# Optimization experiments

Hardware: AMD Instinct MI355X
Metric: run time of the kernel (lower is better)

Reference implementation:

```python
import jax, jax.numpy as jnp
import numpy as np
import math

D_MODEL = 1024
NHEAD = 16
SEQ_LEN = 4096
K_PROJ = 16
HEAD_DIM = D_MODEL // NHEAD


def setup_inputs() -> dict:
    key = jax.random.key(0)
    ks = jax.random.split(key, 11)
    x = jax.random.normal(ks[0], (4, SEQ_LEN, D_MODEL), dtype=jnp.float32)
    s = 1.0 / math.sqrt(D_MODEL)
    Wq = jax.random.uniform(ks[1], (D_MODEL, D_MODEL), minval=-s, maxval=s)
    bq = jax.random.uniform(ks[2], (D_MODEL,), minval=-s, maxval=s)
    Wk = jax.random.uniform(ks[3], (D_MODEL, D_MODEL), minval=-s, maxval=s)
    bk = jax.random.uniform(ks[4], (D_MODEL,), minval=-s, maxval=s)
    Wv = jax.random.uniform(ks[5], (D_MODEL, D_MODEL), minval=-s, maxval=s)
    bv = jax.random.uniform(ks[6], (D_MODEL,), minval=-s, maxval=s)
    Wo = jax.random.uniform(ks[7], (D_MODEL, D_MODEL), minval=-s, maxval=s)
    bo = jax.random.uniform(ks[8], (D_MODEL,), minval=-s, maxval=s)
    E = jax.random.normal(ks[9], (NHEAD, K_PROJ, SEQ_LEN)) * 0.02
    F = jax.random.normal(ks[10], (NHEAD, K_PROJ, SEQ_LEN)) * 0.02
    return {"x": x, "Wq": Wq, "bq": bq, "Wk": Wk, "bk": bk,
            "Wv": Wv, "bv": bv, "Wo": Wo, "bo": bo, "E": E, "F": F}


def reference(x, Wq, bq, Wk, bk, Wv, bv, Wo, bo, E, F):
    B, N, D = x.shape
    # torch Linear: y = x @ W.T + b
    q = x @ Wq.T + bq
    k = x @ Wk.T + bk
    v = x @ Wv.T + bv
    # [B, H, N, Dh]
    def split_heads(t):
        return t.reshape(B, N, NHEAD, HEAD_DIM).transpose(0, 2, 1, 3)
    q, k, v = split_heads(q), split_heads(k), split_heads(v)
    # low-rank projections of K, V along sequence: [B, H, Kp, Dh]
    k_lin = jnp.einsum('bhnd,hkn->bhkd', k, E)
    v_lin = jnp.einsum('bhnd,hkn->bhkd', v, F)
    scores = jnp.einsum('bhnd,bhkd->bhnk', q, k_lin) / math.sqrt(HEAD_DIM)
    attn = jax.nn.softmax(scores, axis=-1)  # dropout is identity in eval
    out = jnp.einsum('bhnk,bhkd->bhnd', attn, v_lin)
    out = out.transpose(0, 2, 1, 3).reshape(B, N, D)
    return out @ Wo.T + bo
```

## Files before the change

### kernel.cpp

```cpp
#include <hip/hip_runtime.h>
#include <hip/hip_bf16.h>

#define SEQLEN 4096

typedef __bf16 bf16x8 __attribute__((ext_vector_type(8)));
typedef float f32x4 __attribute__((ext_vector_type(4)));
typedef __attribute__((ext_vector_type(8))) unsigned short u16x8;

__device__ inline float bf2f(unsigned short s) {
  union { unsigned u; float f; } t; t.u = ((unsigned)s) << 16; return t.f;
}
__device__ inline unsigned short f2bf(float f) {
  __hip_bfloat16 h = __float2bfloat16(f);
  return *reinterpret_cast<unsigned short*>(&h);
}

__device__ inline void gload_lds16(const void* g, void* l) {
  __builtin_amdgcn_global_load_lds(
      (const __attribute__((address_space(1))) unsigned int*)g,
      (__attribute__((address_space(3))) unsigned int*)l, 16, 0, 0);
}

__global__ void cvt_f32_to_bf16(const float* __restrict__ s,
                                unsigned short* __restrict__ d, int n4) {
  int i = blockIdx.x * 256 + threadIdx.x;
  if (i >= n4) return;
  float4 v = reinterpret_cast<const float4*>(s)[i];
  ushort4 o;
  o.x = f2bf(v.x); o.y = f2bf(v.y); o.z = f2bf(v.z); o.w = f2bf(v.w);
  reinterpret_cast<ushort4*>(d)[i] = o;
}

__global__ void pack_bias(const float* __restrict__ a, const float* __restrict__ b,
                          const float* __restrict__ c, float* __restrict__ dst) {
  int i = blockIdx.x * 256 + threadIdx.x;
  if (i < 1024) { dst[i] = a[i]; dst[1024 + i] = b[i]; dst[2048 + i] = c[i]; }
}


#define MFMA16(mk, A00, A01, A10, A11)                                          \
  __builtin_amdgcn_s_setprio(1);                                                \
  _Pragma("unroll")                                                             \
  for (int n = 0; n < 4; ++n) {                                                 \
    acc[2*(mk)][n]   = __builtin_amdgcn_mfma_f32_16x16x32_bf16(A00, b[n][0], acc[2*(mk)][n],   0, 0, 0); \
    acc[2*(mk)][n]   = __builtin_amdgcn_mfma_f32_16x16x32_bf16(A01, b[n][1], acc[2*(mk)][n],   0, 0, 0); \
    acc[2*(mk)+1][n] = __builtin_amdgcn_mfma_f32_16x16x32_bf16(A10, b[n][0], acc[2*(mk)+1][n], 0, 0, 0); \
    acc[2*(mk)+1][n] = __builtin_amdgcn_mfma_f32_16x16x32_bf16(A11, b[n][1], acc[2*(mk)+1][n], 0, 0, 0); \
  }                                                                             \
  __builtin_amdgcn_s_setprio(0);

#define LDA8(mi, sg) (*reinterpret_cast<const bf16x8*>(&as[((wr << 7) + (mi) * 16 + r16) * 64 + (sg) * 8]))
#define LDB8(ni, sg) (*reinterpret_cast<const bf16x8*>(&bs[((wc << 6) + (ni) * 16 + r16) * 64 + (sg) * 8]))

template <typename OUT_T>
__global__ __launch_bounds__(512, 2) void gemm8p(
    const unsigned short* __restrict__ A, const unsigned short* __restrict__ B,
    const float* __restrict__ bias, OUT_T* __restrict__ C, int M, int N, int K,
    int ldc) {
  extern __shared__ __align__(16) unsigned short lds[];

  const int tid = threadIdx.x;
  const int lane = tid & 63, wv = tid >> 6;
  const int wr = wv >> 2, wc = wv & 3;
  const int r16 = lane & 15, kg = lane >> 4;
  const int sg0 = (0 * 4 + kg) ^ (r16 & 7);
  const int sg1 = (1 * 4 + kg) ^ (r16 & 7);

  const int nwg = gridDim.x;
  const int cpx = nwg >> 3;
  const int swz = ((int)blockIdx.x & 7) * cpx + ((int)blockIdx.x >> 3);
  const int mt = M >> 8;
  const int tile_m = swz % mt, tile_n = swz / mt;
  const int brow = tile_m << 8, bcol = tile_n << 8;

  const unsigned short* Ag = A + (size_t)brow * K;
  const unsigned short* Bg = B + (size_t)bcol * K;

  const int sr = tid >> 3;
  const int sc = tid & 7;
  const int sgl = sc ^ (sr & 7);

  auto STG = [&](const unsigned short* G, unsigned short* dstbuf, int row0, int kt) {
    gload_lds16(G + (size_t)(row0 + sr) * K + (size_t)kt * 64 + sgl * 8,
                dstbuf + (row0 + sr) * 64 + sc * 8);
  };

  f32x4 acc[8][4];
#pragma unroll
  for (int m = 0; m < 8; ++m)
#pragma unroll
    for (int n = 0; n < 4; ++n) acc[m][n] = (f32x4)0.0f;

  {
    unsigned short* a0 = lds;
    unsigned short* b0 = lds + 32768;
    STG(Bg, b0, 0, 0);   STG(Bg, b0, 64, 0);
    STG(Bg, b0, 128, 0); STG(Bg, b0, 192, 0);
    STG(Ag, a0, 0, 0);   STG(Ag, a0, 128, 0);
    STG(Ag, a0, 64, 0);  STG(Ag, a0, 192, 0);
  }
  asm volatile("s_waitcnt vmcnt(2)" ::: "memory");
  __builtin_amdgcn_s_barrier();

  const int NT = K >> 6;
  for (int t = 0; t < NT; ++t) {
    const int cur = t & 1;
    const unsigned short* as = lds + (cur << 14);
    const unsigned short* bs = lds + 32768 + (cur << 14);
    unsigned short* an = lds + ((cur ^ 1) << 14);
    unsigned short* bn = lds + 32768 + ((cur ^ 1) << 14);
    const int tn = (t + 1 < NT) ? t + 1 : 0;

    bf16x8 b[4][2];
#pragma unroll
    for (int n = 0; n < 4; ++n) { b[n][0] = LDB8(n, sg0); b[n][1] = LDB8(n, sg1); }

    {
      bf16x8 a00 = LDA8(0, sg0), a01 = LDA8(0, sg1);
      bf16x8 a10 = LDA8(1, sg0), a11 = LDA8(1, sg1);
      STG(Bg, bn, 0, tn);   STG(Bg, bn, 64, tn);
      STG(Bg, bn, 128, tn); STG(Bg, bn, 192, tn);
      __builtin_amdgcn_s_barrier();
      MFMA16(0, a00, a01, a10, a11);
      __builtin_amdgcn_s_barrier();
    }
    {
      bf16x8 a00 = LDA8(2, sg0), a01 = LDA8(2, sg1);
      bf16x8 a10 = LDA8(3, sg0), a11 = LDA8(3, sg1);
      STG(Ag, an, 0, tn); STG(Ag, an, 128, tn);
      __builtin_amdgcn_s_barrier();
      MFMA16(1, a00, a01, a10, a11);
      asm volatile("s_waitcnt vmcnt(6)" ::: "memory");
      __builtin_amdgcn_s_barrier();
    }
    {
      bf16x8 a00 = LDA8(4, sg0), a01 = LDA8(4, sg1);
      bf16x8 a10 = LDA8(5, sg0), a11 = LDA8(5, sg1);
      STG(Ag, an, 64, tn); STG(Ag, an, 192, tn);
      __builtin_amdgcn_s_barrier();
      MFMA16(2, a00, a01, a10, a11);
      __builtin_amdgcn_s_barrier();
    }
    {
      bf16x8 a00 = LDA8(6, sg0), a01 = LDA8(6, sg1);
      bf16x8 a10 = LDA8(7, sg0), a11 = LDA8(7, sg1);
      __builtin_amdgcn_s_barrier();
      MFMA16(3, a00, a01, a10, a11);
      asm volatile("s_waitcnt vmcnt(2)" ::: "memory");
      __builtin_amdgcn_s_barrier();
    }
  }
  asm volatile("s_waitcnt vmcnt(0)" ::: "memory");

  if constexpr (sizeof(OUT_T) == 2) {
    __builtin_amdgcn_s_barrier();
    unsigned short* C2 = reinterpret_cast<unsigned short*>(C);
    float bvs[4];
#pragma unroll
    for (int n = 0; n < 4; ++n)
      bvs[n] = bias ? bias[bcol + wc * 64 + n * 16 + r16] : 0.0f;
#pragma unroll
    for (int m = 0; m < 8; ++m) {
#pragma unroll
      for (int r = 0; r < 4; ++r) {
        int rw = m * 16 + kg * 4 + r;
        int xo = (rw & 12) << 2;
#pragma unroll
        for (int n = 0; n < 4; ++n) {
          lds[wv * 8192 + rw * 64 + ((n * 16 + r16) ^ xo)] =
              f2bf(acc[m][n][r] + bvs[n]);
        }
      }
    }
    __syncthreads();
#pragma unroll
    for (int p = 0; p < 16; ++p) {
      int grow = p * 16 + (tid >> 5);
      int g = tid & 31;
      int wvs = ((grow >> 7) << 2) + (g >> 3);
      int row_l = grow & 127;
      int src = wvs * 8192 + row_l * 64 + (((g & 7) * 8) ^ ((row_l & 12) << 2));
      u16x8 vv = *reinterpret_cast<const u16x8*>(&lds[src]);
      *reinterpret_cast<u16x8*>(&C2[(size_t)(brow + grow) * ldc + bcol + g * 8]) = vv;
    }
  } else {
#pragma unroll
    for (int n = 0; n < 4; ++n) {
      int col = bcol + wc * 64 + n * 16 + r16;
      float bv = bias ? bias[col] : 0.0f;
#pragma unroll
      for (int m = 0; m < 8; ++m) {
#pragma unroll
        for (int r = 0; r < 4; ++r) {
          int row = brow + wr * 128 + m * 16 + kg * 4 + r;
          C[(size_t)row * ldc + col] = acc[m][n][r] + bv;
        }
      }
    }
  }
}

__global__ void kvlin_part(const unsigned short* __restrict__ qkv,
                           const float* __restrict__ E, const float* __restrict__ F,
                           float* __restrict__ part) {
  __shared__ __align__(16) unsigned short Ks[128 * 64], Vs[128 * 64];
  __shared__ __align__(16) float Es[16 * 128], Fs[16 * 128];
  const int tid = threadIdx.x;
  const int bid = blockIdx.x;
  const int bh = bid >> 3, ns = bid & 7;
  const int b = bh >> 4, h = bh & 15;
  const int d = tid & 63, kk = tid >> 6;
  float aK[4] = {0, 0, 0, 0}, aV[4] = {0, 0, 0, 0};
  for (int c = 0; c < 4; ++c) {
    int n0 = ns * 512 + c * 128;
#pragma unroll
    for (int it = 0; it < 4; ++it) {
      int f = it * 256 + tid;
      int row = f >> 3, ch = f & 7;
      const unsigned short* gk =
          qkv + (size_t)(b * SEQLEN + n0 + row) * 3072 + 1024 + h * 64 + ch * 8;
      gload_lds16(gk, &Ks[f * 8]);
      gload_lds16(gk + 1024, &Vs[f * 8]);
    }
#pragma unroll
    for (int it = 0; it < 2; ++it) {
      int f = it * 256 + tid;
      int k = f >> 5, ch = f & 31;
      const float* ge = E + (size_t)(h * 16 + k) * SEQLEN + n0 + ch * 4;
      const float* gf = F + (size_t)(h * 16 + k) * SEQLEN + n0 + ch * 4;
      gload_lds16(ge, &Es[f * 4]);
      gload_lds16(gf, &Fs[f * 4]);
    }
    __syncthreads();
    for (int n = 0; n < 128; ++n) {
      float kv = bf2f(Ks[n * 64 + d]);
      float vv = bf2f(Vs[n * 64 + d]);
#pragma unroll
      for (int j = 0; j < 4; ++j) {
        aK[j] += Es[(kk * 4 + j) * 128 + n] * kv;
        aV[j] += Fs[(kk * 4 + j) * 128 + n] * vv;
      }
    }
    __syncthreads();
  }
  size_t base = ((size_t)ns * 64 + bh) * 2048;
#pragma unroll
  for (int j = 0; j < 4; ++j) {
    part[base + (kk * 4 + j) * 64 + d] = aK[j];
    part[base + 1024 + (kk * 4 + j) * 64 + d] = aV[j];
  }
}

__global__ void kvlin_reduce(const float* __restrict__ part, float* __restrict__ out) {
  int i = blockIdx.x * 256 + threadIdx.x;
  float s = 0;
#pragma unroll
  for (int ns = 0; ns < 8; ++ns) s += part[(size_t)ns * 131072 + i];
  out[i] = s;
}

__global__ void attn_kernel(const unsigned short* __restrict__ qkv,
                            const float* __restrict__ kvlin,
                            unsigned short* __restrict__ aout) {
  __shared__ float kl[1024], vl[1024];
  const int tid = threadIdx.x;
  const int bid = blockIdx.x;
  const int bh = bid >> 4, nt = bid & 15;
  const int b = bh >> 4, h = bh & 15;
  for (int i = tid; i < 1024; i += 256) {
    kl[i] = kvlin[(size_t)bh * 2048 + i];
    vl[i] = kvlin[(size_t)bh * 2048 + 1024 + i];
  }
  __syncthreads();
  const int n = nt * 256 + tid;
  const unsigned short* qp = qkv + (size_t)(b * SEQLEN + n) * 3072 + h * 64;
  float q[64];
#pragma unroll
  for (int c2 = 0; c2 < 8; ++c2) {
    u16x8 v = *reinterpret_cast<const u16x8*>(qp + c2 * 8);
#pragma unroll
    for (int j = 0; j < 8; ++j) q[c2 * 8 + j] = bf2f(v[j]);
  }
  float s[16];
#pragma unroll
  for (int k = 0; k < 16; ++k) {
    float a = 0;
#pragma unroll
    for (int dd = 0; dd < 64; ++dd) a += q[dd] * kl[k * 64 + dd];
    s[k] = a * 0.125f;
  }
  float mx = s[0];
#pragma unroll
  for (int k = 1; k < 16; ++k) mx = fmaxf(mx, s[k]);
  float sum = 0;
#pragma unroll
  for (int k = 0; k < 16; ++k) { s[k] = __expf(s[k] - mx); sum += s[k]; }
  float inv = 1.0f / sum;
#pragma unroll
  for (int k = 0; k < 16; ++k) s[k] *= inv;
  unsigned short* op = aout + (size_t)(b * SEQLEN + n) * 1024 + h * 64;
#pragma unroll
  for (int d0 = 0; d0 < 8; ++d0) {
    float o[8] = {0, 0, 0, 0, 0, 0, 0, 0};
#pragma unroll
    for (int k = 0; k < 16; ++k) {
      float p = s[k];
#pragma unroll
      for (int j = 0; j < 8; ++j) o[j] += p * vl[k * 64 + d0 * 8 + j];
    }
    u16x8 pk;
#pragma unroll
    for (int j = 0; j < 8; ++j) pk[j] = f2bf(o[j]);
    *reinterpret_cast<u16x8*>(op + d0 * 8) = pk;
  }
}

extern "C" void kernel_launch(void* const* d_in, const int* in_sizes, int n_in,
                              void* d_out, int out_size, void* d_ws, size_t ws_size,
                              hipStream_t stream) {
  const float* x  = (const float*)d_in[0];
  const float* Wq = (const float*)d_in[1];
  const float* bq = (const float*)d_in[2];
  const float* Wk = (const float*)d_in[3];
  const float* bk = (const float*)d_in[4];
  const float* Wv = (const float*)d_in[5];
  const float* bv = (const float*)d_in[6];
  const float* Wo = (const float*)d_in[7];
  const float* bo = (const float*)d_in[8];
  const float* E  = (const float*)d_in[9];
  const float* F  = (const float*)d_in[10];
  float* out = (float*)d_out;

  char* ws = (char*)d_ws;
  unsigned short* Xb   = (unsigned short*)(ws);
  unsigned short* Wqkv = (unsigned short*)(ws + 33554432);
  unsigned short* WoB  = (unsigned short*)(ws + 39845888);
  float*          Bqkv = (float*)(ws + 41943040);
  unsigned short* QKV  = (unsigned short*)(ws + 41955328);
  float*          KVp  = (float*)(ws + 142618624);
  float*          KVl  = (float*)(ws + 146812928);
  unsigned short* AOut = Xb;

  (void)hipFuncSetAttribute(reinterpret_cast<const void*>(gemm8p<unsigned short>),
                            hipFuncAttributeMaxDynamicSharedMemorySize, 131072);
  (void)hipFuncSetAttribute(reinterpret_cast<const void*>(gemm8p<float>),
                            hipFuncAttributeMaxDynamicSharedMemorySize, 131072);

  cvt_f32_to_bf16<<<16384, 256, 0, stream>>>(x, Xb, 4194304);
  cvt_f32_to_bf16<<<1024, 256, 0, stream>>>(Wq, Wqkv, 262144);
  cvt_f32_to_bf16<<<1024, 256, 0, stream>>>(Wk, Wqkv + 1048576, 262144);
  cvt_f32_to_bf16<<<1024, 256, 0, stream>>>(Wv, Wqkv + 2097152, 262144);
  cvt_f32_to_bf16<<<1024, 256, 0, stream>>>(Wo, WoB, 262144);
  pack_bias<<<4, 256, 0, stream>>>(bq, bk, bv, Bqkv);

  gemm8p<unsigned short><<<768, 512, 131072, stream>>>(
      Xb, Wqkv, Bqkv, QKV, 16384, 3072, 1024, 3072);

  kvlin_part<<<512, 256, 0, stream>>>(QKV, E, F, KVp);
  kvlin_reduce<<<512, 256, 0, stream>>>(KVp, KVl);
  attn_kernel<<<1024, 256, 0, stream>>>(QKV, KVl, AOut);

  gemm8p<float><<<256, 512, 131072, stream>>>(
      AOut, WoB, bo, out, 16384, 1024, 1024, 1024);
}
```

Baseline: 266.8 us.

## Fuse conversion kernels, reorder MFMA issue, and remap GEMM tiles per XCD

Merges the five fp32-to-bf16 conversion launches and the bias packing into one kernel, removing several small launches and their gaps. Reorders the MFMA sequence in the GEMM inner macro so that consecutive instructions write different accumulators, which may reduce dependency stalls. Changes the block-to-tile mapping so each XCD handles a contiguous band of M tiles, aiming for better L2 reuse of A rows. The fused kernel adds branching, and the new mapping assumes M/256 is divisible by 8.

```diff
diff --git a/kernel.cpp b/kernel.cpp
--- a/kernel.cpp
+++ b/kernel.cpp
@@ -21,32 +21,59 @@
       (__attribute__((address_space(3))) unsigned int*)l, 16, 0, 0);
 }
 
-__global__ void cvt_f32_to_bf16(const float* __restrict__ s,
-                                unsigned short* __restrict__ d, int n4) {
-  int i = blockIdx.x * 256 + threadIdx.x;
-  if (i >= n4) return;
-  float4 v = reinterpret_cast<const float4*>(s)[i];
+__global__ void cvt_all(const float* __restrict__ x, const float* __restrict__ Wq,
+                        const float* __restrict__ Wk, const float* __restrict__ Wv,
+                        const float* __restrict__ Wo,
+                        const float* __restrict__ bq, const float* __restrict__ bk,
+                        const float* __restrict__ bv,
+                        unsigned short* __restrict__ Xb,
+                        unsigned short* __restrict__ Wqkv,
+                        unsigned short* __restrict__ WoB, float* __restrict__ Bqkv) {
+  long i = (long)blockIdx.x * 256 + threadIdx.x;
+  const float* src;
+  unsigned short* dst;
+  long rel;
+  if (i < 4194304) {
+    src = x; dst = Xb; rel = i;
+  } else if (i < 4456448) {
+    src = Wq; dst = Wqkv; rel = i - 4194304;
+  } else if (i < 4718592) {
+    src = Wk; dst = Wqkv + 1048576; rel = i - 4456448;
+  } else if (i < 4980736) {
+    src = Wv; dst = Wqkv + 2097152; rel = i - 4718592;
+  } else if (i < 5242880) {
+    src = Wo; dst = WoB; rel = i - 4980736;
+  } else if (i < 5243648) {
+    long j = i - 5242880;
+    const float* bsrc = (j < 256) ? bq : (j < 512) ? bk : bv;
+    long jr = j & 255;
+    reinterpret_cast<float4*>(Bqkv)[j] =
+        reinterpret_cast<const float4*>(bsrc)[jr];
+    return;
+  } else {
+    return;
+  }
+  float4 v = reinterpret_cast<const float4*>(src)[rel];
   ushort4 o;
   o.x = f2bf(v.x); o.y = f2bf(v.y); o.z = f2bf(v.z); o.w = f2bf(v.w);
-  reinterpret_cast<ushort4*>(d)[i] = o;
-}
-
-__global__ void pack_bias(const float* __restrict__ a, const float* __restrict__ b,
-                          const float* __restrict__ c, float* __restrict__ dst) {
-  int i = blockIdx.x * 256 + threadIdx.x;
-  if (i < 1024) { dst[i] = a[i]; dst[1024 + i] = b[i]; dst[2048 + i] = c[i]; }
+  reinterpret_cast<ushort4*>(dst)[rel] = o;
 }
 
 
 #define MFMA16(mk, A00, A01, A10, A11)                                          \
   __builtin_amdgcn_s_setprio(1);                                                \
   _Pragma("unroll")                                                             \
-  for (int n = 0; n < 4; ++n) {                                                 \
+  for (int n = 0; n < 4; ++n)                                                   \
     acc[2*(mk)][n]   = __builtin_amdgcn_mfma_f32_16x16x32_bf16(A00, b[n][0], acc[2*(mk)][n],   0, 0, 0); \
+  _Pragma("unroll")                                                             \
+  for (int n = 0; n < 4; ++n)                                                   \
+    acc[2*(mk)+1][n] = __builtin_amdgcn_mfma_f32_16x16x32_bf16(A10, b[n][0], acc[2*(mk)+1][n], 0, 0, 0); \
+  _Pragma("unroll")                                                             \
+  for (int n = 0; n < 4; ++n)                                                   \
     acc[2*(mk)][n]   = __builtin_amdgcn_mfma_f32_16x16x32_bf16(A01, b[n][1], acc[2*(mk)][n],   0, 0, 0); \
-    acc[2*(mk)+1][n] = __builtin_amdgcn_mfma_f32_16x16x32_bf16(A10, b[n][0], acc[2*(mk)+1][n], 0, 0, 0); \
+  _Pragma("unroll")                                                             \
+  for (int n = 0; n < 4; ++n)                                                   \
     acc[2*(mk)+1][n] = __builtin_amdgcn_mfma_f32_16x16x32_bf16(A11, b[n][1], acc[2*(mk)+1][n], 0, 0, 0); \
-  }                                                                             \
   __builtin_amdgcn_s_setprio(0);
 
 #define LDA8(mi, sg) (*reinterpret_cast<const bf16x8*>(&as[((wr << 7) + (mi) * 16 + r16) * 64 + (sg) * 8]))
@@ -66,11 +93,11 @@
   const int sg0 = (0 * 4 + kg) ^ (r16 & 7);
   const int sg1 = (1 * 4 + kg) ^ (r16 & 7);
 
-  const int nwg = gridDim.x;
-  const int cpx = nwg >> 3;
-  const int swz = ((int)blockIdx.x & 7) * cpx + ((int)blockIdx.x >> 3);
-  const int mt = M >> 8;
-  const int tile_m = swz % mt, tile_n = swz / mt;
+  const int xcd = (int)blockIdx.x & 7;
+  const int pos = (int)blockIdx.x >> 3;
+  const int rpx = (M >> 8) >> 3;
+  const int tile_m = xcd * rpx + (pos % rpx);
+  const int tile_n = pos / rpx;
   const int brow = tile_m << 8, bcol = tile_n << 8;
 
   const unsigned short* Ag = A + (size_t)brow * K;
@@ -346,12 +373,8 @@
   (void)hipFuncSetAttribute(reinterpret_cast<const void*>(gemm8p<float>),
                             hipFuncAttributeMaxDynamicSharedMemorySize, 131072);
 
-  cvt_f32_to_bf16<<<16384, 256, 0, stream>>>(x, Xb, 4194304);
-  cvt_f32_to_bf16<<<1024, 256, 0, stream>>>(Wq, Wqkv, 262144);
-  cvt_f32_to_bf16<<<1024, 256, 0, stream>>>(Wk, Wqkv + 1048576, 262144);
-  cvt_f32_to_bf16<<<1024, 256, 0, stream>>>(Wv, Wqkv + 2097152, 262144);
-  cvt_f32_to_bf16<<<1024, 256, 0, stream>>>(Wo, WoB, 262144);
-  pack_bias<<<4, 256, 0, stream>>>(bq, bk, bv, Bqkv);
+  cvt_all<<<20483, 256, 0, stream>>>(x, Wq, Wk, Wv, Wo, bq, bk, bv,
+                                     Xb, Wqkv, WoB, Bqkv);
 
   gemm8p<unsigned short><<<768, 512, 131072, stream>>>(
       Xb, Wqkv, Bqkv, QKV, 16384, 3072, 1024, 3072);
```

New measurement: 253.4 us. 5.0% less time.
